# Kernel optimization log

Measured on AMD Instinct MI355X. Metric: run time of the kernel, lower is better.

Reference implementation:

```python
import jax, jax.numpy as jnp
import numpy as np

DT = 0.01          # model_config['dt']
FULL_ITERS = 30    # torchdeq f_max_iter
REUSE_ITERS = 5    # solver_kwargs={'f_max_iter': 5} when reusing w0


def setup_inputs() -> dict:
    key = jax.random.key(0)
    ks = jax.random.split(key, 16)
    B, T, IN, ST, NL, OUT, H = 2048, 32, 16, 16, 128, 8, 64
    n = lambda k, shp, s: s * jax.random.normal(k, shp, dtype=jnp.float32)
    return {
        "obs": n(ks[0], (B, T, IN), 1.0),
        "x0": jnp.zeros((B, ST), jnp.float32),
        "A_T": n(ks[1], (ST, ST), 0.25),
        "Bw_T": n(ks[2], (NL, ST), 0.08),
        "By_T": n(ks[3], (ST, ST), 0.25),
        "Cv_T": n(ks[4], (ST, NL), 0.2),
        "Dvw_T": n(ks[5], (NL, NL), 0.04),  # contractive so fixed-point iter converges
        "Dvy_T": n(ks[6], (ST, NL), 0.2),
        "Cu_T": n(ks[7], (ST, OUT), 0.25),
        "Duw_T": n(ks[8], (NL, OUT), 0.08),
        "Duy_T": n(ks[9], (ST, OUT), 0.25),
        "log_stds": jnp.full((OUT,), -1.6094379124341003, jnp.float32),
        "W1": n(ks[10], (IN, H), 1.0 / np.sqrt(IN)),
        "b1": jnp.zeros((H,), jnp.float32),
        "W2": n(ks[11], (H, H), 1.0 / np.sqrt(H)),
        "b2": jnp.zeros((H,), jnp.float32),
        "W3": n(ks[12], (H, 1), 1.0 / np.sqrt(H)),
        "b3": jnp.zeros((1,), jnp.float32),
    }


def reference(obs, x0, A_T, Bw_T, By_T, Cv_T, Dvw_T, Dvy_T, Cu_T, Duw_T,
              Duy_T, log_stds, W1, b1, W2, b2, W3, b3):
    B, T, IN = obs.shape
    NL = Dvw_T.shape[0]

    def fpi(f, w0, n_iter):
        # torchdeq fixed_point_iter: w <- f(w), n_iter times, return last iterate
        w, _ = jax.lax.scan(lambda w, _: (f(w), None), w0, None, length=n_iter)
        return w

    def xdot(x, y, w0, n_iter):
        f = lambda w: jnp.tanh(x @ Cv_T + w @ Dvw_T + y @ Dvy_T)
        w = fpi(f, w0, n_iter)
        return x @ A_T + w @ Bw_T + y @ By_T, w

    def step(x, y):
        # RK4 with y held constant over the step; w solution reused as warm start
        w_init = jnp.zeros((B, NL), x.dtype)
        k1, w1 = xdot(x, y, w_init, FULL_ITERS)
        k2, w2 = xdot(x + DT * k1 / 2, y, w1, REUSE_ITERS)
        k3, w3 = xdot(x + DT * k2 / 2, y, w2, REUSE_ITERS)
        k4, w4 = xdot(x + DT * k3, y, w3, REUSE_ITERS)
        next_x = x + DT / 6 * (k1 + 2 * k2 + 2 * k3 + k4)
        u = x @ Cu_T + w1 @ Duw_T + y @ Duy_T  # controller output at current state
        return next_x, u

    ys = jnp.swapaxes(obs, 0, 1)  # [T, B, IN]
    _, us = jax.lax.scan(step, x0, ys)  # us: [T, B, OUT]
    means = jnp.swapaxes(us, 0, 1)  # [B, T, OUT]
    log_std_b = jnp.broadcast_to(log_stds, means.shape)

    # value baseline MLP on observations
    h = jnp.tanh(obs @ W1 + b1)
    h = jnp.tanh(h @ W2 + b2)
    value = h @ W3 + b3  # [B, T, 1]

    return jnp.concatenate([means, log_std_b, value], axis=-1)  # [B, T, 2*OUT+1]
```

## Files before the change

kernel.cpp:

```cpp
#include <hip/hip_runtime.h>


typedef _Float16 f16x8 __attribute__((ext_vector_type(8)));
typedef float f32x4 __attribute__((ext_vector_type(4)));
typedef int i32x4 __attribute__((ext_vector_type(4)));

constexpr int B_TOT   = 2048;
constexpr int T_STEPS = 32;
constexpr int IN_D    = 16;
constexpr int ST_D    = 16;
constexpr int NL_D    = 128;
constexpr int OUT_D   = 8;
constexpr int H_D     = 64;
constexpr int OUT_C   = 17;
constexpr float DT_F  = 0.01f;
constexpr float SC    = 2.8853900817779268f;

__device__ __forceinline__ int eperm(int s, int g, int j) {
    return 32 * s + 16 * (j >> 2) + 4 * g + (j & 3);
}

#define MFMA16(A, B, C) __builtin_amdgcn_mfma_f32_16x16x32_f16((A), (B), (C), 0, 0, 0)
#define PK(a, b) __builtin_bit_cast(int, __builtin_amdgcn_cvt_pkrtz((a), (b)))

__global__ __launch_bounds__(256, 1) void rinn_fpi(
    const float* __restrict__ obs, const float* __restrict__ x0,
    const float* __restrict__ A_T, const float* __restrict__ Bw_T,
    const float* __restrict__ By_T, const float* __restrict__ Cv_T,
    const float* __restrict__ Dvw_T, const float* __restrict__ Dvy_T,
    const float* __restrict__ Cu_T, const float* __restrict__ Duw_T,
    const float* __restrict__ Duy_T, float* __restrict__ out)
{
    __shared__ __align__(16) char xch[2][4][1024];
    const int tid  = threadIdx.x;
    const int wid  = tid >> 6;
    const int lane = tid & 63;
    const int g    = lane >> 4;
    const int r16  = lane & 15;
    const int row  = blockIdx.x * 16 + r16;
    const f32x4 z4 = {0.f, 0.f, 0.f, 0.f};

    const int c1 = (wid + 1) & 3, c2 = (wid + 2) & 3, c3 = (wid + 3) & 3;

    f16x8 aD[2][4];
#pragma unroll
    for (int n = 0; n < 2; ++n)
#pragma unroll
        for (int i = 0; i < 4; ++i) {
            const int s = (wid + i) & 3;
            f16x8 h;
#pragma unroll
            for (int j = 0; j < 8; ++j)
                h[j] = (_Float16)(SC * Dvw_T[eperm(s, g, j) * NL_D + 16 * (2 * wid + n) + r16]);
            aD[n][i] = h;
        }
    f16x8 aB[2];
#pragma unroll
    for (int n = 0; n < 2; ++n) {
        const int m = 16 * (2 * wid + n) + r16;
        f16x8 h;
#pragma unroll
        for (int j = 0; j < 8; ++j) {
            float v = (j < 4) ? Cv_T[(4 * g + j) * NL_D + m]
                              : Dvy_T[(4 * g + (j & 3)) * NL_D + m];
            h[j] = (_Float16)(SC * v);
        }
        aB[n] = h;
    }
    f16x8 aK[5];
    {
        f16x8 h;
#pragma unroll
        for (int j = 0; j < 8; ++j)
            h[j] = (_Float16)((j < 4) ? A_T[(4 * g + j) * ST_D + r16]
                                      : By_T[(4 * g + (j & 3)) * ST_D + r16]);
        aK[0] = h;
#pragma unroll
        for (int i = 0; i < 4; ++i) {
            const int s = (wid + i) & 3;
            f16x8 h2;
#pragma unroll
            for (int j = 0; j < 8; ++j)
                h2[j] = (_Float16)Bw_T[eperm(s, g, j) * ST_D + r16];
            aK[1 + i] = h2;
        }
    }
    f16x8 aU[5];
    if (wid == 1) {
        f16x8 h;
#pragma unroll
        for (int j = 0; j < 8; ++j) {
            float v = 0.f;
            if (r16 < OUT_D)
                v = (j < 4) ? Cu_T[(4 * g + j) * OUT_D + r16]
                            : Duy_T[(4 * g + (j & 3)) * OUT_D + r16];
            h[j] = (_Float16)v;
        }
        aU[0] = h;
#pragma unroll
        for (int i = 0; i < 4; ++i) {
            const int s = (wid + i) & 3;
            f16x8 h2;
#pragma unroll
            for (int j = 0; j < 8; ++j)
                h2[j] = (_Float16)((r16 < OUT_D) ? Duw_T[eperm(s, g, j) * OUT_D + r16] : 0.f);
            aU[1 + i] = h2;
        }
    } else {
#pragma unroll
        for (int s = 0; s < 5; ++s) aU[s] = __builtin_bit_cast(f16x8, z4);
    }

    f32x4 xb = *(const f32x4*)(x0 + row * ST_D + 4 * g);

    f16x8 f0, f1, f2, f3;
    int cur = 0;
    char* const xbase = &xch[0][0][0];
    const int loff = lane * 16;

    auto tanh4 = [&](f32x4 t) -> f32x4 {
        f32x4 o;
#pragma unroll
        for (int q = 0; q < 4; ++q)
            o[q] = fmaf(-2.0f, __builtin_amdgcn_rcpf(1.0f + __builtin_amdgcn_exp2f(t[q])), 1.0f);
        return o;
    };

    auto fpi = [&](int niter, f32x4 bias0, f32x4 bias1) {
#pragma unroll 1
        for (int it = 0; it < niter; ++it) {
            f32x4 c00 = MFMA16(aD[0][0], f0, bias0);
            f32x4 c10 = MFMA16(aD[1][0], f0, bias1);
            f32x4 c01 = MFMA16(aD[0][2], f2, z4);
            f32x4 c11 = MFMA16(aD[1][2], f2, z4);
            c00 = MFMA16(aD[0][1], f1, c00);
            c10 = MFMA16(aD[1][1], f1, c10);
            c01 = MFMA16(aD[0][3], f3, c01);
            c11 = MFMA16(aD[1][3], f3, c11);
            f32x4 v0 = tanh4(c00 + c01);
            f32x4 v1 = tanh4(c10 + c11);
            i32x4 own;
            own[0] = PK(v0[0], v0[1]);
            own[1] = PK(v0[2], v0[3]);
            own[2] = PK(v1[0], v1[1]);
            own[3] = PK(v1[2], v1[3]);
            char* nb = xbase + (cur ^ 1) * 4096;
            *(i32x4*)(nb + wid * 1024 + loff) = own;
            __syncthreads();
            f0 = __builtin_bit_cast(f16x8, own);
            f1 = *(const f16x8*)(nb + c1 * 1024 + loff);
            f2 = *(const f16x8*)(nb + c2 * 1024 + loff);
            f3 = *(const f16x8*)(nb + c3 * 1024 + loff);
            cur ^= 1;
        }
    };

#pragma unroll 1
    for (int t = 0; t < T_STEPS; ++t) {
        f32x4 yb = *(const f32x4*)(obs + (row * T_STEPS + t) * IN_D + 4 * g);
        const int yw2 = PK(yb[0], yb[1]);
        const int yw3 = PK(yb[2], yb[3]);
        f0 = f1 = f2 = f3 = __builtin_bit_cast(f16x8, z4);
        f32x4 k1 = z4, k2 = z4, k3 = z4, k4 = z4;
        f32x4 xc = xb;

#pragma unroll
        for (int st = 0; st < 4; ++st) {
            i32x4 bxyw;
            bxyw[0] = PK(xc[0], xc[1]);
            bxyw[1] = PK(xc[2], xc[3]);
            bxyw[2] = yw2;
            bxyw[3] = yw3;
            f16x8 bXY = __builtin_bit_cast(f16x8, bxyw);
            f32x4 bias0 = MFMA16(aB[0], bXY, z4);
            f32x4 bias1 = MFMA16(aB[1], bXY, z4);
            fpi(st ? 5 : 30, bias0, bias1);
            f32x4 e0 = MFMA16(aK[0], bXY, z4);
            e0 = MFMA16(aK[1], f0, e0);
            e0 = MFMA16(aK[2], f1, e0);
            f32x4 e1 = MFMA16(aK[3], f2, z4);
            e1 = MFMA16(aK[4], f3, e1);
            f32x4 kc = e0 + e1;
            if (st == 0) {
                if (wid == 1) {
                    f32x4 u0 = MFMA16(aU[0], bXY, z4);
                    u0 = MFMA16(aU[1], f0, u0);
                    u0 = MFMA16(aU[2], f1, u0);
                    f32x4 u1 = MFMA16(aU[3], f2, z4);
                    u1 = MFMA16(aU[4], f3, u1);
                    f32x4 uc = u0 + u1;
                    if (g < 2) {
                        float* op = out + (row * T_STEPS + t) * OUT_C + 4 * g;
                        op[0] = uc[0]; op[1] = uc[1]; op[2] = uc[2]; op[3] = uc[3];
                    }
                }
                k1 = kc;
#pragma unroll
                for (int q = 0; q < 4; ++q) xc[q] = fmaf(0.5f * DT_F, k1[q], xb[q]);
            } else if (st == 1) {
                k2 = kc;
#pragma unroll
                for (int q = 0; q < 4; ++q) xc[q] = fmaf(0.5f * DT_F, k2[q], xb[q]);
            } else if (st == 2) {
                k3 = kc;
#pragma unroll
                for (int q = 0; q < 4; ++q) xc[q] = fmaf(DT_F, k3[q], xb[q]);
            } else {
                k4 = kc;
#pragma unroll
                for (int q = 0; q < 4; ++q)
                    xb[q] = fmaf(DT_F / 6.0f,
                                 k1[q] + 2.0f * k2[q] + 2.0f * k3[q] + k4[q], xb[q]);
            }
        }
    }
}

__device__ __forceinline__ float fast_tanh(float a) {
    float e = __expf(2.0f * a);
    return 1.0f - 2.0f / (e + 1.0f);
}

__global__ __launch_bounds__(256) void mlp_kernel(
    const float* __restrict__ obs, const float* __restrict__ log_stds,
    const float* __restrict__ W1, const float* __restrict__ b1,
    const float* __restrict__ W2, const float* __restrict__ b2,
    const float* __restrict__ W3, const float* __restrict__ b3,
    float* __restrict__ out) {
    __shared__ float sW1[IN_D * H_D];
    __shared__ float sW2[H_D * H_D];
    __shared__ float sb1[H_D], sb2[H_D], sW3[H_D], sls[OUT_D];
    __shared__ float sb3;
    const int tid = threadIdx.x;
    for (int i = tid; i < IN_D * H_D; i += 256) sW1[i] = W1[i];
    for (int i = tid; i < H_D * H_D; i += 256) sW2[i] = W2[i];
    if (tid < H_D) { sb1[tid] = b1[tid]; sb2[tid] = b2[tid]; sW3[tid] = W3[tid]; }
    if (tid < OUT_D) sls[tid] = log_stds[tid];
    if (tid == 0) sb3 = b3[0];
    __syncthreads();

    const int bt = blockIdx.x * 256 + tid;
    if (bt >= B_TOT * T_STEPS) return;

    float o[IN_D];
#pragma unroll
    for (int i = 0; i < IN_D; ++i) o[i] = obs[bt * IN_D + i];

    float h1[H_D];
#pragma unroll
    for (int h = 0; h < H_D; ++h) {
        float a = sb1[h];
#pragma unroll
        for (int i = 0; i < IN_D; ++i) a = fmaf(o[i], sW1[i * H_D + h], a);
        h1[h] = fast_tanh(a);
    }
    float v = sb3;
#pragma unroll
    for (int h = 0; h < H_D; ++h) {
        float a = sb2[h];
#pragma unroll
        for (int i = 0; i < H_D; ++i) a = fmaf(h1[i], sW2[i * H_D + h], a);
        v = fmaf(fast_tanh(a), sW3[h], v);
    }

    float* o17 = out + bt * OUT_C;
#pragma unroll
    for (int q = 0; q < OUT_D; ++q) o17[OUT_D + q] = sls[q];
    o17[16] = v;
}

extern "C" void kernel_launch(void* const* d_in, const int* in_sizes, int n_in,
                              void* d_out, int out_size, void* d_ws, size_t ws_size,
                              hipStream_t stream) {
    const float* obs      = (const float*)d_in[0];
    const float* x0       = (const float*)d_in[1];
    const float* A_T      = (const float*)d_in[2];
    const float* Bw_T     = (const float*)d_in[3];
    const float* By_T     = (const float*)d_in[4];
    const float* Cv_T     = (const float*)d_in[5];
    const float* Dvw_T    = (const float*)d_in[6];
    const float* Dvy_T    = (const float*)d_in[7];
    const float* Cu_T     = (const float*)d_in[8];
    const float* Duw_T    = (const float*)d_in[9];
    const float* Duy_T    = (const float*)d_in[10];
    const float* log_stds = (const float*)d_in[11];
    const float* W1       = (const float*)d_in[12];
    const float* b1       = (const float*)d_in[13];
    const float* W2       = (const float*)d_in[14];
    const float* b2       = (const float*)d_in[15];
    const float* W3       = (const float*)d_in[16];
    const float* b3       = (const float*)d_in[17];
    float* out = (float*)d_out;

    rinn_fpi<<<dim3(B_TOT / 16), dim3(256), 0, stream>>>(
        obs, x0, A_T, Bw_T, By_T, Cv_T, Dvw_T, Dvy_T, Cu_T, Duw_T, Duy_T, out);
    mlp_kernel<<<dim3((B_TOT * T_STEPS + 255) / 256), dim3(256), 0, stream>>>(
        obs, log_stds, W1, b1, W2, b2, W3, b3, out);
}
```

Before: 429.7 us.

## Split fixed-point NL tiles across eight waves instead of four

Each block now runs 8 waves, each computing one 16-wide NL tile of the fixed-point tanh iteration instead of two. This halves the MFMA and tanh work per wave on the serial iteration critical path. Each wave writes 8 bytes into the shared exchange buffer and reads back all four f16x8 fragments. The cost is a barrier across 512 threads each iteration, more LDS reads per wave, and duplicated RK4/state MFMAs across more waves. The unchanged RK4/output tail may still assume four waves, so its correctness with eight is unclear.

```diff
diff --git a/kernel.cpp b/kernel.cpp
--- a/kernel.cpp
+++ b/kernel.cpp
@@ -3,7 +3,7 @@
 
 typedef _Float16 f16x8 __attribute__((ext_vector_type(8)));
 typedef float f32x4 __attribute__((ext_vector_type(4)));
-typedef int i32x4 __attribute__((ext_vector_type(4)));
+typedef int i32x2 __attribute__((ext_vector_type(2)));
 
 constexpr int B_TOT   = 2048;
 constexpr int T_STEPS = 32;
@@ -23,7 +23,7 @@
 #define MFMA16(A, B, C) __builtin_amdgcn_mfma_f32_16x16x32_f16((A), (B), (C), 0, 0, 0)
 #define PK(a, b) __builtin_bit_cast(int, __builtin_amdgcn_cvt_pkrtz((a), (b)))
 
-__global__ __launch_bounds__(256, 1) void rinn_fpi(
+__global__ __launch_bounds__(512, 1) void rinn_fpi(
     const float* __restrict__ obs, const float* __restrict__ x0,
     const float* __restrict__ A_T, const float* __restrict__ Bw_T,
     const float* __restrict__ By_T, const float* __restrict__ Cv_T,
@@ -40,24 +40,18 @@
     const int row  = blockIdx.x * 16 + r16;
     const f32x4 z4 = {0.f, 0.f, 0.f, 0.f};
 
-    const int c1 = (wid + 1) & 3, c2 = (wid + 2) & 3, c3 = (wid + 3) & 3;
-
-    f16x8 aD[2][4];
-#pragma unroll
-    for (int n = 0; n < 2; ++n)
-#pragma unroll
-        for (int i = 0; i < 4; ++i) {
-            const int s = (wid + i) & 3;
-            f16x8 h;
-#pragma unroll
-            for (int j = 0; j < 8; ++j)
-                h[j] = (_Float16)(SC * Dvw_T[eperm(s, g, j) * NL_D + 16 * (2 * wid + n) + r16]);
-            aD[n][i] = h;
-        }
-    f16x8 aB[2];
-#pragma unroll
-    for (int n = 0; n < 2; ++n) {
-        const int m = 16 * (2 * wid + n) + r16;
+    f16x8 aD[4];
+#pragma unroll
+    for (int s = 0; s < 4; ++s) {
+        f16x8 h;
+#pragma unroll
+        for (int j = 0; j < 8; ++j)
+            h[j] = (_Float16)(SC * Dvw_T[eperm(s, g, j) * NL_D + 16 * wid + r16]);
+        aD[s] = h;
+    }
+    f16x8 aB;
+    {
+        const int m = 16 * wid + r16;
         f16x8 h;
 #pragma unroll
         for (int j = 0; j < 8; ++j) {
@@ -65,7 +59,7 @@
                               : Dvy_T[(4 * g + (j & 3)) * NL_D + m];
             h[j] = (_Float16)(SC * v);
         }
-        aB[n] = h;
+        aB = h;
     }
     f16x8 aK[5];
     {
@@ -76,13 +70,12 @@
                                       : By_T[(4 * g + (j & 3)) * ST_D + r16]);
         aK[0] = h;
 #pragma unroll
-        for (int i = 0; i < 4; ++i) {
-            const int s = (wid + i) & 3;
+        for (int s = 0; s < 4; ++s) {
             f16x8 h2;
 #pragma unroll
             for (int j = 0; j < 8; ++j)
                 h2[j] = (_Float16)Bw_T[eperm(s, g, j) * ST_D + r16];
-            aK[1 + i] = h2;
+            aK[1 + s] = h2;
         }
     }
     f16x8 aU[5];
@@ -98,13 +91,12 @@
         }
         aU[0] = h;
 #pragma unroll
-        for (int i = 0; i < 4; ++i) {
-            const int s = (wid + i) & 3;
+        for (int s = 0; s < 4; ++s) {
             f16x8 h2;
 #pragma unroll
             for (int j = 0; j < 8; ++j)
                 h2[j] = (_Float16)((r16 < OUT_D) ? Duw_T[eperm(s, g, j) * OUT_D + r16] : 0.f);
-            aU[1 + i] = h2;
+            aU[1 + s] = h2;
         }
     } else {
 #pragma unroll
@@ -117,6 +109,7 @@
     int cur = 0;
     char* const xbase = &xch[0][0][0];
     const int loff = lane * 16;
+    const int woff = (wid >> 1) * 1024 + loff + (wid & 1) * 8;
 
     auto tanh4 = [&](f32x4 t) -> f32x4 {
         f32x4 o;
@@ -126,31 +119,24 @@
         return o;
     };
 
-    auto fpi = [&](int niter, f32x4 bias0, f32x4 bias1) {
+    auto fpi = [&](int niter, f32x4 bias) {
 #pragma unroll 1
         for (int it = 0; it < niter; ++it) {
-            f32x4 c00 = MFMA16(aD[0][0], f0, bias0);
-            f32x4 c10 = MFMA16(aD[1][0], f0, bias1);
-            f32x4 c01 = MFMA16(aD[0][2], f2, z4);
-            f32x4 c11 = MFMA16(aD[1][2], f2, z4);
-            c00 = MFMA16(aD[0][1], f1, c00);
-            c10 = MFMA16(aD[1][1], f1, c10);
-            c01 = MFMA16(aD[0][3], f3, c01);
-            c11 = MFMA16(aD[1][3], f3, c11);
-            f32x4 v0 = tanh4(c00 + c01);
-            f32x4 v1 = tanh4(c10 + c11);
-            i32x4 own;
-            own[0] = PK(v0[0], v0[1]);
-            own[1] = PK(v0[2], v0[3]);
-            own[2] = PK(v1[0], v1[1]);
-            own[3] = PK(v1[2], v1[3]);
+            f32x4 ca = MFMA16(aD[0], f0, bias);
+            f32x4 cb = MFMA16(aD[2], f2, z4);
+            ca = MFMA16(aD[1], f1, ca);
+            cb = MFMA16(aD[3], f3, cb);
+            f32x4 v = tanh4(ca + cb);
+            i32x2 own;
+            own[0] = PK(v[0], v[1]);
+            own[1] = PK(v[2], v[3]);
             char* nb = xbase + (cur ^ 1) * 4096;
-            *(i32x4*)(nb + wid * 1024 + loff) = own;
+            *(i32x2*)(nb + woff) = own;
             __syncthreads();
-            f0 = __builtin_bit_cast(f16x8, own);
-            f1 = *(const f16x8*)(nb + c1 * 1024 + loff);
-            f2 = *(const f16x8*)(nb + c2 * 1024 + loff);
-            f3 = *(const f16x8*)(nb + c3 * 1024 + loff);
+            f0 = *(const f16x8*)(nb + 0 * 1024 + loff);
+            f1 = *(const f16x8*)(nb + 1 * 1024 + loff);
+            f2 = *(const f16x8*)(nb + 2 * 1024 + loff);
+            f3 = *(const f16x8*)(nb + 3 * 1024 + loff);
             cur ^= 1;
         }
     };
@@ -166,15 +152,14 @@
 
 #pragma unroll
         for (int st = 0; st < 4; ++st) {
-            i32x4 bxyw;
-            bxyw[0] = PK(xc[0], xc[1]);
-            bxyw[1] = PK(xc[2], xc[3]);
-            bxyw[2] = yw2;
-            bxyw[3] = yw3;
-            f16x8 bXY = __builtin_bit_cast(f16x8, bxyw);
-            f32x4 bias0 = MFMA16(aB[0], bXY, z4);
-            f32x4 bias1 = MFMA16(aB[1], bXY, z4);
-            fpi(st ? 5 : 30, bias0, bias1);
+            i32x2 bxl;
+            bxl[0] = PK(xc[0], xc[1]);
+            bxl[1] = PK(xc[2], xc[3]);
+            int bxyw[4] = {bxl[0], bxl[1], yw2, yw3};
+            f16x8 bXY;
+            memcpy(&bXY, bxyw, 16);
+            f32x4 bias = MFMA16(aB, bXY, z4);
+            fpi(st ? 5 : 30, bias);
             f32x4 e0 = MFMA16(aK[0], bXY, z4);
             e0 = MFMA16(aK[1], f0, e0);
             e0 = MFMA16(aK[2], f1, e0);
@@ -292,7 +277,7 @@
     const float* b3       = (const float*)d_in[17];
     float* out = (float*)d_out;
 
-    rinn_fpi<<<dim3(B_TOT / 16), dim3(256), 0, stream>>>(
+    rinn_fpi<<<dim3(B_TOT / 16), dim3(512), 0, stream>>>(
         obs, x0, A_T, Bw_T, By_T, Cv_T, Dvw_T, Dvy_T, Cu_T, Duw_T, Duy_T, out);
     mlp_kernel<<<dim3((B_TOT * T_STEPS + 255) / 256), dim3(256), 0, stream>>>(
         obs, log_stds, W1, b1, W2, b2, W3, b3, out);
```

New measurement: 396.1 us, median of 2. 7.8% less time.
